# Kernel tuning notes

Hardware: AMD Instinct MI355X
Metric: run time of the kernel (lower is better)

## Reference

```python
import jax, jax.numpy as jnp
import numpy as np

D_MODEL, D_INNER, D_STATE, DT_RANK, USERS = 2560, 5120, 16, 160, 32

def setup_inputs() -> dict:
    key = jax.random.key(0)
    ks = jax.random.split(key, 16)
    s = lambda k, shp, sc=0.02: (jax.random.normal(k, shp, dtype=jnp.float32) * sc)
    return {
        "x": jax.random.normal(ks[0], (1, 1, USERS, D_MODEL), dtype=jnp.float32),
        "w_in_ssm": s(ks[1], (D_MODEL, D_INNER)),
        "w_in_mlp": s(ks[2], (D_MODEL, D_INNER)),
        "w_out": s(ks[3], (D_INNER, D_MODEL)),
        "conv_w": s(ks[4], (4, D_INNER), 0.5),
        "conv_b": s(ks[5], (D_INNER,), 0.1),
        "conv_state1": jax.random.normal(ks[6], (1, 1, USERS, D_INNER), dtype=jnp.float32),
        "conv_state2": jax.random.normal(ks[7], (1, 1, USERS, D_INNER), dtype=jnp.float32),
        "conv_state3": jax.random.normal(ks[8], (1, 1, USERS, D_INNER), dtype=jnp.float32),
        "x_proj_w": s(ks[9], (D_INNER, DT_RANK + 2 * D_STATE)),
        "dt_proj_w": s(ks[10], (DT_RANK, D_INNER)),
        "dt_proj_b": s(ks[11], (D_INNER,), 0.1),
        "A_log": jax.random.uniform(ks[12], (D_INNER, D_STATE), dtype=jnp.float32),
        "D_param": s(ks[13], (D_INNER,), 1.0),
        "ssm_state": jax.random.normal(ks[14], (USERS, D_INNER, D_STATE), dtype=jnp.float32) * 0.1,
    }

def reference(x, w_in_ssm, w_in_mlp, w_out, conv_w, conv_b,
              conv_state1, conv_state2, conv_state3,
              x_proj_w, dt_proj_w, dt_proj_b, A_log, D_param, ssm_state):
    xb = x.reshape(USERS, D_MODEL)                       # [U, d_model]
    xs = xb @ w_in_ssm                                    # [U, d_inner] (newest conv tap)
    # 4-tap depthwise causal conv via shifted state buffer (unrolled in original)
    taps = (conv_state1.reshape(USERS, D_INNER),
            conv_state2.reshape(USERS, D_INNER),
            conv_state3.reshape(USERS, D_INNER),
            xs)
    c = taps[0] * conv_w[0] + taps[1] * conv_w[1] + taps[2] * conv_w[2] + taps[3] * conv_w[3] + conv_b
    c = jax.nn.silu(c)                                    # [U, d_inner]
    # selective SSM single-step update
    x_dbl = c @ x_proj_w                                  # [U, dt_rank + 2*d_state]
    dt = jax.nn.softplus(x_dbl[:, :DT_RANK] @ dt_proj_w + dt_proj_b)   # [U, d_inner]
    B = x_dbl[:, DT_RANK:DT_RANK + D_STATE]               # [U, d_state]
    C = x_dbl[:, DT_RANK + D_STATE:]                      # [U, d_state]
    A = -jnp.exp(A_log)                                   # [d_inner, d_state]
    dA = jnp.exp(dt[:, :, None] * A[None])                # [U, d_inner, d_state]
    new_state = ssm_state * dA + (dt * c)[:, :, None] * B[:, None, :]
    y = jnp.einsum("uds,us->ud", new_state, C) + D_param * c           # [U, d_inner]
    res = xb @ w_in_mlp                                   # gate branch (no extra silu, per source)
    out = (y * res) @ w_out                               # [U, d_model]
    return out.reshape(1, 1, USERS, D_MODEL)
```

## Files before the change

kernel.cpp:

```cpp
#include <hip/hip_runtime.h>
#include <hip/hip_bf16.h>
#include <cstdint>
#include <cstddef>

#define U   32
#define DM  2560
#define DI  5120
#define DS  16
#define RNK 160
#define XD  192
#define KC1 16
#define KC4 64

typedef __attribute__((ext_vector_type(8)))  short bf16x8;
typedef __attribute__((ext_vector_type(16))) float f32x16;

__device__ __forceinline__ unsigned int pkbf(float a, float b) {
  __hip_bfloat162 h = __float22bfloat162_rn(make_float2(a, b));
  union { __hip_bfloat162 h; unsigned int u; } v; v.h = h; return v.u;
}
__device__ __forceinline__ unsigned short f2bfu(float f) {
  __hip_bfloat16 h = __float2bfloat16(f);
  union { __hip_bfloat16 h; unsigned short u; } v; v.h = h; return v.u;
}
__device__ __forceinline__ float bf2f(unsigned int s) {
  union { float f; unsigned int u; } v; v.u = s << 16; return v.f;
}

__device__ __forceinline__ void gl_lds16(const float* g, float* l) {
  __builtin_amdgcn_global_load_lds(
      (const __attribute__((address_space(1))) unsigned int*)g,
      (__attribute__((address_space(3))) unsigned int*)l,
      16, 0, 2 );
}

template<int LDW, int SLAB>
__global__ __launch_bounds__(256, 3) void skinny_dma(
    const float* __restrict__ A, int lda,
    const float* __restrict__ W0, const float* __restrict__ W1,
    unsigned short* __restrict__ part)
{
  constexpr int NS = SLAB / 16;
  __shared__ float        wbuf[2][16][256];
  __shared__ unsigned int albuf[NS][64][4];

  const int tid  = threadIdx.x;
  const int lane = tid & 63, w = tid >> 6;
  const int kcb  = blockIdx.y, z = blockIdx.z;
  const int k0   = kcb * SLAB;
  const float* __restrict__ W = z ? W1 : W0;
  const int col0 = blockIdx.x * 256;

  for (int i = tid; i < U * (SLAB / 2); i += 256) {
    const int u  = i / (SLAB / 2);
    const int kp = i - u * (SLAB / 2);
    const int k  = 2 * kp;
    const float2 v = *(const float2*)&A[(size_t)u * lda + k0 + k];
    albuf[k >> 4][u + U * ((k >> 3) & 1)][(k >> 1) & 3] = pkbf(v.x, v.y);
  }

  const int cl = lane & 31, half = lane >> 5;

  {
    const float* src = W + ((size_t)k0 + w * 4) * LDW + col0 + lane * 4;
#pragma unroll
    for (int i = 0; i < 4; ++i)
      gl_lds16(src + (size_t)i * LDW, &wbuf[0][w * 4 + i][0]);
  }

  f32x16 acc0{}, acc1{};

  for (int s = 0; s < NS; ++s) {
    const int buf = s & 1;
    if (s + 1 < NS) {
      const float* src = W + ((size_t)k0 + (s + 1) * 16 + w * 4) * LDW
                         + col0 + lane * 4;
#pragma unroll
      for (int i = 0; i < 4; ++i)
        gl_lds16(src + (size_t)i * LDW, &wbuf[buf ^ 1][w * 4 + i][0]);
    }
    __syncthreads();

    bf16x8 af = *(const bf16x8*)&albuf[s][lane][0];
#pragma unroll
    for (int f = 0; f < 2; ++f) {
      const int col = w * 64 + f * 32 + cl;
      float r0 = wbuf[buf][half * 8 + 0][col];
      float r1 = wbuf[buf][half * 8 + 1][col];
      float r2 = wbuf[buf][half * 8 + 2][col];
      float r3 = wbuf[buf][half * 8 + 3][col];
      float r4 = wbuf[buf][half * 8 + 4][col];
      float r5 = wbuf[buf][half * 8 + 5][col];
      float r6 = wbuf[buf][half * 8 + 6][col];
      float r7 = wbuf[buf][half * 8 + 7][col];
      union { bf16x8 v; unsigned int d[4]; } bu;
      bu.d[0] = pkbf(r0, r1); bu.d[1] = pkbf(r2, r3);
      bu.d[2] = pkbf(r4, r5); bu.d[3] = pkbf(r6, r7);
      if (f == 0) acc0 = __builtin_amdgcn_mfma_f32_32x32x16_bf16(af, bu.v, acc0, 0, 0, 0);
      else        acc1 = __builtin_amdgcn_mfma_f32_32x32x16_bf16(af, bu.v, acc1, 0, 0, 0);
    }
    __syncthreads();
  }

  unsigned short* po = part + (size_t)(z * gridDim.y + kcb) * U * LDW + col0;
#pragma unroll
  for (int f = 0; f < 2; ++f) {
    const f32x16& a = f ? acc1 : acc0;
    const int gc = w * 64 + f * 32 + cl;
#pragma unroll
    for (int r = 0; r < 16; ++r) {
      const int m = (r & 3) + 8 * (r >> 2) + 4 * half;
      po[(size_t)m * LDW + gc] = f2bfu(a[r]);
    }
  }
}

__global__ __launch_bounds__(256) void k2a_convsilu(
    const unsigned short* __restrict__ part,
    const float* __restrict__ cs1, const float* __restrict__ cs2,
    const float* __restrict__ cs3,
    const float* __restrict__ cw,  const float* __restrict__ cb,
    float* __restrict__ c_ws, float* __restrict__ res_ws,
    float* __restrict__ x_dbl)
{
  const int t = blockIdx.x * 256 + threadIdx.x;
  if (t < U * XD / 2) *(float2*)&x_dbl[2 * t] = make_float2(0.f, 0.f);

  const int i = 2 * t;
  const int u = i / DI, d = i - u * DI;
  float xs0 = 0.f, xs1 = 0.f, rs0 = 0.f, rs1 = 0.f;
#pragma unroll 4
  for (int kc = 0; kc < KC1; ++kc) {
    unsigned int a = *(const unsigned int*)&part[((size_t)kc * U + u) * DI + d];
    unsigned int b = *(const unsigned int*)&part[((size_t)(KC1 + kc) * U + u) * DI + d];
    xs0 += bf2f(a & 0xffffu); xs1 += bf2f(a >> 16);
    rs0 += bf2f(b & 0xffffu); rs1 += bf2f(b >> 16);
  }
  const float2 s1 = *(const float2*)&cs1[i];
  const float2 s2 = *(const float2*)&cs2[i];
  const float2 s3 = *(const float2*)&cs3[i];
  const float2 w0 = *(const float2*)&cw[d];
  const float2 w1 = *(const float2*)&cw[DI + d];
  const float2 w2 = *(const float2*)&cw[2 * DI + d];
  const float2 w3 = *(const float2*)&cw[3 * DI + d];
  const float2 bb = *(const float2*)&cb[d];
  float c0 = s1.x * w0.x + s2.x * w1.x + s3.x * w2.x + xs0 * w3.x + bb.x;
  float c1 = s1.y * w0.y + s2.y * w1.y + s3.y * w2.y + xs1 * w3.y + bb.y;
  c0 = c0 / (1.f + __expf(-c0));
  c1 = c1 / (1.f + __expf(-c1));
  *(float2*)&c_ws[i]   = make_float2(c0, c1);
  *(float2*)&res_ws[i] = make_float2(rs0, rs1);
}

__global__ __launch_bounds__(256) void k2b_xproj(
    const float* __restrict__ c_ws,
    const float* __restrict__ xpw,
    float* __restrict__ x_dbl)
{
  __shared__ union { float ct[U][80]; float red[4][64][33]; } sh;
  const int k0 = blockIdx.y * 80;

  for (int i4 = threadIdx.x; i4 < U * 20; i4 += 256) {
    int u = i4 / 20, k4 = i4 - u * 20;
    *(float4*)&sh.ct[u][k4 * 4] = *(const float4*)&c_ws[u * DI + k0 + k4 * 4];
  }
  __syncthreads();

  const int c = threadIdx.x & 63, s = threadIdx.x >> 6;
  const int col = blockIdx.x * 64 + c;
  const float* Wp = xpw + (size_t)(k0 + s * 20) * XD + col;

  float acc[U];
#pragma unroll
  for (int u = 0; u < U; ++u) acc[u] = 0.f;

  for (int kk = 0; kk < 20; kk += 4) {
    float w0 = Wp[(size_t)(kk + 0) * XD];
    float w1 = Wp[(size_t)(kk + 1) * XD];
    float w2 = Wp[(size_t)(kk + 2) * XD];
    float w3 = Wp[(size_t)(kk + 3) * XD];
#pragma unroll
    for (int u = 0; u < U; ++u) {
      float4 cv = *(const float4*)&sh.ct[u][s * 20 + kk];
      acc[u] = fmaf(cv.x, w0, acc[u]);
      acc[u] = fmaf(cv.y, w1, acc[u]);
      acc[u] = fmaf(cv.z, w2, acc[u]);
      acc[u] = fmaf(cv.w, w3, acc[u]);
    }
  }

  __syncthreads();
#pragma unroll
  for (int u = 0; u < U; ++u) sh.red[s][c][u] = acc[u];
  __syncthreads();

  for (int p = threadIdx.x; p < 64 * U; p += 256) {
    int cc = p & 63, u = p >> 6;
    float v = sh.red[0][cc][u] + sh.red[1][cc][u] + sh.red[2][cc][u] + sh.red[3][cc][u];
    atomicAdd(&x_dbl[u * XD + blockIdx.x * 64 + cc], v);
  }
}

__global__ __launch_bounds__(256) void k3_fused(
    const float* __restrict__ x_dbl,
    const float* __restrict__ dpw, const float* __restrict__ dpb,
    const float* __restrict__ alog, const float* __restrict__ Dp,
    const float* __restrict__ ssm,
    const float* __restrict__ c_ws, const float* __restrict__ res_ws,
    float* __restrict__ yr)
{
  __shared__ union { float xt[U][160]; float red[4][64][33]; } sh;
  __shared__ float dtl[U][64];
  __shared__ float bc[U][32];

  const int tid = threadIdx.x, bx = blockIdx.x;

  for (int i4 = tid; i4 < U * 40; i4 += 256) {
    int u = i4 / 40, r4 = i4 - u * 40;
    *(float4*)&sh.xt[u][r4 * 4] = *(const float4*)&x_dbl[u * XD + r4 * 4];
  }
  for (int i = tid; i < U * 32; i += 256) {
    int u = i >> 5, j = i & 31;
    bc[u][j] = x_dbl[u * XD + RNK + j];
  }
  __syncthreads();

  const int c = tid & 63, s = tid >> 6;
  const int d = bx * 64 + c;
  const float* Wp = dpw + (size_t)(s * 40) * DI + d;

  float acc[U];
#pragma unroll
  for (int u = 0; u < U; ++u) acc[u] = 0.f;

  for (int rr = 0; rr < 40; rr += 4) {
    float w0 = Wp[(size_t)(rr + 0) * DI];
    float w1 = Wp[(size_t)(rr + 1) * DI];
    float w2 = Wp[(size_t)(rr + 2) * DI];
    float w3 = Wp[(size_t)(rr + 3) * DI];
#pragma unroll
    for (int u = 0; u < U; ++u) {
      float4 xv = *(const float4*)&sh.xt[u][s * 40 + rr];
      acc[u] = fmaf(xv.x, w0, acc[u]);
      acc[u] = fmaf(xv.y, w1, acc[u]);
      acc[u] = fmaf(xv.z, w2, acc[u]);
      acc[u] = fmaf(xv.w, w3, acc[u]);
    }
  }

  __syncthreads();
#pragma unroll
  for (int u = 0; u < U; ++u) sh.red[s][c][u] = acc[u];
  __syncthreads();

  for (int p = tid; p < 64 * U; p += 256) {
    int cc = p & 63, u = p >> 6;
    float pre = sh.red[0][cc][u] + sh.red[1][cc][u] + sh.red[2][cc][u] + sh.red[3][cc][u]
              + dpb[bx * 64 + cc];
    dtl[u][cc] = fmaxf(pre, 0.f) + log1pf(expf(-fabsf(pre)));
  }
  __syncthreads();

  for (int p = tid; p < 64 * U; p += 256) {
    const int cc = p & 63, u = p >> 6;
    const int dg = bx * 64 + cc;
    const int i  = u * DI + dg;
    const float dt = dtl[u][cc];
    const float cv = c_ws[i];
    const float rv = res_ws[i];
    const float Dv = Dp[dg];
    const float dtc = dt * cv;

    const float* st = ssm + ((size_t)u * DI + dg) * DS;
    float y = 0.f;
#pragma unroll
    for (int q = 0; q < 4; ++q) {
      float4 al = *(const float4*)&alog[dg * DS + q * 4];
      float4 sv = *(const float4*)&st[q * 4];
      y += (sv.x * __expf(dt * -__expf(al.x)) + dtc * bc[u][q * 4 + 0]) * bc[u][16 + q * 4 + 0];
      y += (sv.y * __expf(dt * -__expf(al.y)) + dtc * bc[u][q * 4 + 1]) * bc[u][16 + q * 4 + 1];
      y += (sv.z * __expf(dt * -__expf(al.z)) + dtc * bc[u][q * 4 + 2]) * bc[u][16 + q * 4 + 2];
      y += (sv.w * __expf(dt * -__expf(al.w)) + dtc * bc[u][q * 4 + 3]) * bc[u][16 + q * 4 + 3];
    }
    y = fmaf(Dv, cv, y);
    yr[i] = y * rv;
  }
}

__global__ __launch_bounds__(256) void k5_reduce(
    const unsigned short* __restrict__ part4,
    float* __restrict__ out)
{
  const int t = blockIdx.x * 256 + threadIdx.x;
  const int i = 2 * t;
  const int u = i / DM, d = i - u * DM;
  float v0 = 0.f, v1 = 0.f;
#pragma unroll 8
  for (int kc = 0; kc < KC4; ++kc) {
    unsigned int a = *(const unsigned int*)&part4[((size_t)kc * U + u) * DM + d];
    v0 += bf2f(a & 0xffffu);
    v1 += bf2f(a >> 16);
  }
  *(float2*)&out[i] = make_float2(v0, v1);
}

extern "C" void kernel_launch(void* const* d_in, const int* in_sizes, int n_in,
                              void* d_out, int out_size, void* d_ws, size_t ws_size,
                              hipStream_t stream)
{
  const float* x    = (const float*)d_in[0];
  const float* wssm = (const float*)d_in[1];
  const float* wmlp = (const float*)d_in[2];
  const float* wout = (const float*)d_in[3];
  const float* cw   = (const float*)d_in[4];
  const float* cb   = (const float*)d_in[5];
  const float* cs1  = (const float*)d_in[6];
  const float* cs2  = (const float*)d_in[7];
  const float* cs3  = (const float*)d_in[8];
  const float* xpw  = (const float*)d_in[9];
  const float* dpw  = (const float*)d_in[10];
  const float* dpb  = (const float*)d_in[11];
  const float* alog = (const float*)d_in[12];
  const float* Dp   = (const float*)d_in[13];
  const float* ssm  = (const float*)d_in[14];
  float* out = (float*)d_out;

  unsigned short* partb = (unsigned short*)d_ws;
  float* c_ws   = (float*)(partb + (size_t)2 * KC1 * U * DI);
  float* res_ws = c_ws   + (size_t)U * DI;
  float* yrb    = res_ws + (size_t)U * DI;
  float* x_dbl  = yrb    + (size_t)U * DI;

  skinny_dma<DI, 160><<<dim3(20, KC1, 2), 256, 0, stream>>>(x, DM, wssm, wmlp, partb);
  k2a_convsilu<<<320, 256, 0, stream>>>(partb, cs1, cs2, cs3, cw, cb, c_ws, res_ws, x_dbl);
  k2b_xproj<<<dim3(3, 64), 256, 0, stream>>>(c_ws, xpw, x_dbl);
  k3_fused<<<80, 256, 0, stream>>>(x_dbl, dpw, dpb, alog, Dp, ssm, c_ws, res_ws, yrb);
  skinny_dma<DM, 80><<<dim3(10, KC4, 1), 256, 0, stream>>>(yrb, DI, wout, wout, partb);
  k5_reduce<<<160, 256, 0, stream>>>(partb, out);
}
```

Baseline: 84.33 us.

## Add register-pipelined first GEMM kernel and retune split-K chunking

```diff
diff --git a/kernel.cpp b/kernel.cpp
--- a/kernel.cpp
+++ b/kernel.cpp
@@ -9,8 +9,8 @@
 #define DS  16
 #define RNK 160
 #define XD  192
-#define KC1 16
-#define KC4 64
+#define KC1 20
+#define KC4 32
 
 typedef __attribute__((ext_vector_type(8)))  short bf16x8;
 typedef __attribute__((ext_vector_type(16))) float f32x16;
@@ -31,7 +31,101 @@
   __builtin_amdgcn_global_load_lds(
       (const __attribute__((address_space(1))) unsigned int*)g,
       (__attribute__((address_space(3))) unsigned int*)l,
-      16, 0, 2 );
+      16, 0, 0);
+}
+
+template<int LDW, int CHUNK>
+__global__ __launch_bounds__(256, 4) void k1_deep(
+    const float* __restrict__ A, int lda,
+    const float* __restrict__ W0, const float* __restrict__ W1,
+    unsigned short* __restrict__ part)
+{
+  constexpr int NS = CHUNK / 16;
+  __shared__ unsigned int albuf[NS][65][4];
+  __shared__ unsigned int bbuf[4][8][64];
+
+  const int tid  = threadIdx.x;
+  const int lane = tid & 63, w = tid >> 6;
+  const int kcb  = blockIdx.y, z = blockIdx.z;
+  const int k0   = kcb * CHUNK;
+  const float* __restrict__ W = z ? W1 : W0;
+  const int col0 = blockIdx.x * 256 + w * 64;
+
+  for (int i = tid; i < U * (CHUNK / 2); i += 256) {
+    const int u  = i / (CHUNK / 2);
+    const int kp = i - u * (CHUNK / 2);
+    const int k  = 2 * kp;
+    const float2 v = *(const float2*)&A[(size_t)u * lda + k0 + k];
+    albuf[k >> 4][u + U * ((k >> 3) & 1)][(k >> 1) & 3] = pkbf(v.x, v.y);
+  }
+  __syncthreads();
+
+  const int cq  = (lane & 15) * 4;
+  const int rp0 = lane >> 4;
+  const int cl  = lane & 31, half = lane >> 5;
+
+  const float* wp = W + (size_t)k0 * LDW + col0 + cq;
+  const size_t rA = (size_t)(2 * rp0) * LDW;
+  const size_t rB = rA + LDW;
+  const size_t rC = (size_t)(2 * rp0 + 8) * LDW;
+  const size_t rD = rC + LDW;
+
+  f32x16 acc0{}, acc1{};
+
+#define LOADP(P, S)                                                       \
+  P##A = *(const float4*)(wp + (size_t)(S) * 16 * LDW + rA);              \
+  P##B = *(const float4*)(wp + (size_t)(S) * 16 * LDW + rB);              \
+  P##C = *(const float4*)(wp + (size_t)(S) * 16 * LDW + rC);              \
+  P##D = *(const float4*)(wp + (size_t)(S) * 16 * LDW + rD);
+
+#define CONS(P, S)                                                        \
+  {                                                                       \
+    uint4 dA, dB;                                                         \
+    dA.x = pkbf(P##A.x, P##B.x); dA.y = pkbf(P##A.y, P##B.y);             \
+    dA.z = pkbf(P##A.z, P##B.z); dA.w = pkbf(P##A.w, P##B.w);             \
+    dB.x = pkbf(P##C.x, P##D.x); dB.y = pkbf(P##C.y, P##D.y);             \
+    dB.z = pkbf(P##C.z, P##D.z); dB.w = pkbf(P##C.w, P##D.w);             \
+    *(uint4*)&bbuf[w][rp0][cq]     = dA;                                  \
+    *(uint4*)&bbuf[w][rp0 + 4][cq] = dB;                                  \
+    bf16x8 af = *(const bf16x8*)&albuf[S][lane][0];                       \
+    union { bf16x8 v; unsigned int d[4]; } b0, b1;                        \
+    _Pragma("unroll")                                                     \
+    for (int q = 0; q < 4; ++q) {                                         \
+      b0.d[q] = bbuf[w][half * 4 + q][cl];                                \
+      b1.d[q] = bbuf[w][half * 4 + q][cl + 32];                           \
+    }                                                                     \
+    acc0 = __builtin_amdgcn_mfma_f32_32x32x16_bf16(af, b0.v, acc0, 0,0,0);\
+    acc1 = __builtin_amdgcn_mfma_f32_32x32x16_bf16(af, b1.v, acc1, 0,0,0);\
+  }
+
+  float4 p0A, p0B, p0C, p0D, p1A, p1B, p1C, p1D, p2A, p2B, p2C, p2D;
+
+  LOADP(p0, 0) LOADP(p1, 1) LOADP(p2, 2)
+  CONS(p0, 0) LOADP(p0, 3)
+  CONS(p1, 1) LOADP(p1, 4)
+  CONS(p2, 2) LOADP(p2, 5)
+  CONS(p0, 3) LOADP(p0, 6)
+  CONS(p1, 4) LOADP(p1, 7)
+  CONS(p2, 5)
+  CONS(p0, 6)
+  CONS(p1, 7)
+  static_assert(NS == 8, "pipeline is unrolled for NS==8");
+
+#undef LOADP
+#undef CONS
+
+  unsigned short* po = part + (size_t)(z * gridDim.y + kcb) * U * LDW
+                       + blockIdx.x * 256 + w * 64;
+#pragma unroll
+  for (int f = 0; f < 2; ++f) {
+    const f32x16& a = f ? acc1 : acc0;
+    const int gc = f * 32 + cl;
+#pragma unroll
+    for (int r = 0; r < 16; ++r) {
+      const int m = (r & 3) + 8 * (r >> 2) + 4 * half;
+      po[(size_t)m * LDW + gc] = f2bfu(a[r]);
+    }
+  }
 }
 
 template<int LDW, int SLAB>
@@ -331,10 +425,10 @@
   float* yrb    = res_ws + (size_t)U * DI;
   float* x_dbl  = yrb    + (size_t)U * DI;
 
-  skinny_dma<DI, 160><<<dim3(20, KC1, 2), 256, 0, stream>>>(x, DM, wssm, wmlp, partb);
+  k1_deep<DI, 128><<<dim3(20, KC1, 2), 256, 0, stream>>>(x, DM, wssm, wmlp, partb);
   k2a_convsilu<<<320, 256, 0, stream>>>(partb, cs1, cs2, cs3, cw, cb, c_ws, res_ws, x_dbl);
   k2b_xproj<<<dim3(3, 64), 256, 0, stream>>>(c_ws, xpw, x_dbl);
   k3_fused<<<80, 256, 0, stream>>>(x_dbl, dpw, dpb, alog, Dp, ssm, c_ws, res_ws, yrb);
-  skinny_dma<DM, 80><<<dim3(10, KC4, 1), 256, 0, stream>>>(yrb, DI, wout, wout, partb);
+  skinny_dma<DM, 160><<<dim3(10, KC4, 1), 256, 0, stream>>>(yrb, DI, wout, wout, partb);
   k5_reduce<<<160, 256, 0, stream>>>(partb, out);
 }
```

Result: faster. 78.37 us (-7.1%).
